# Kernel optimization log

Hardware: AMD Instinct MI355X
Metric: run time of the kernel (lower is better)

Reference implementation:

```python
import jax, jax.numpy as jnp
import numpy as np

B, L, VOCAB = 32768, 512, 50000
CROP_RATIO, MIN_LEN = 0.8, 3
MASK_RATIO, MASK_TOKEN = 0.2, 0
REORDER_RATIO, MIN_W, MAX_W = 0.3, 2, 5


def setup_inputs() -> dict:
    key = jax.random.key(0)
    k1, k2 = jax.random.split(key)
    lens = jax.random.randint(k1, (B,), 1, L + 1)
    items = jax.random.randint(k2, (B, L), 1, VOCAB)
    pos = jnp.arange(L)[None, :]
    item_seq = jnp.where(pos < lens[:, None], items, 0).astype(jnp.int32)
    return {"item_seq": item_seq, "item_seq_len": lens.astype(jnp.int32)}


def _mask_aug(key, seq, lens):
    pos = jnp.arange(seq.shape[1])[None, :]
    valid = (pos < lens[:, None]) & (seq != 0)
    n_valid = valid.sum(axis=1)
    n_mask = jnp.minimum(jnp.maximum(1, (n_valid * MASK_RATIO).astype(jnp.int32)), n_valid)
    scores = jnp.where(valid, jax.random.uniform(key, seq.shape), jnp.inf)
    # rank of each position among valid positions by random score
    rank = jnp.argsort(jnp.argsort(scores, axis=1), axis=1)
    apply_row = (lens > 1) & (n_valid > 0)
    do_mask = valid & (rank < n_mask[:, None]) & apply_row[:, None]
    return jnp.where(do_mask, MASK_TOKEN, seq), lens


def _crop_aug(key, seq, lens):
    Lm = seq.shape[1]
    crop_len = jnp.minimum(jnp.maximum(MIN_LEN, (lens * CROP_RATIO).astype(jnp.int32)), lens)
    max_start = jnp.maximum(lens - crop_len + 1, 1)
    start = (jax.random.uniform(key, (seq.shape[0],)) * max_start).astype(jnp.int32)
    pos = jnp.arange(Lm)[None, :]
    idx = jnp.minimum(start[:, None] + pos, Lm - 1)
    cropped = jnp.where(pos < crop_len[:, None], jnp.take_along_axis(seq, idx, axis=1), 0)
    apply_row = lens > MIN_LEN
    return (jnp.where(apply_row[:, None], cropped, seq),
            jnp.where(apply_row, crop_len, lens))


def _reorder_aug(key, seq, lens):
    Bm, Lm = seq.shape
    k1, k2, k3, k4 = jax.random.split(key, 4)
    pos = jnp.arange(Lm)[None, :]
    valid = (pos < lens[:, None]) & (seq != 0)
    n_valid = valid.sum(axis=1)
    # valid positions first (in order), padding positions after
    valid_idx = jnp.argsort(jnp.where(valid, pos, Lm + pos), axis=1)
    max_w = jnp.minimum(n_valid, MAX_W)
    wsize = MIN_W + (jax.random.uniform(k1, (Bm,)) * jnp.maximum(max_w - MIN_W + 1, 1)).astype(jnp.int32)
    wsize = jnp.clip(wsize, MIN_W, MAX_W)
    max_start = jnp.maximum(n_valid - wsize + 1, 1)
    start = (jax.random.uniform(k2, (Bm,)) * max_start).astype(jnp.int32)
    apply_row = (lens > MIN_W) & (jax.random.uniform(k3, (Bm,)) <= REORDER_RATIO) & (n_valid >= MIN_W)
    k = jnp.arange(MAX_W)[None, :]
    slot_ok = k < wsize[:, None]
    win_cols = jnp.take_along_axis(valid_idx, jnp.minimum(start[:, None] + k, Lm - 1), axis=1)
    win_items = jnp.take_along_axis(seq, win_cols, axis=1)
    # random permutation within the (ragged) window via sorted random keys
    keys = jnp.where(slot_ok, jax.random.uniform(k4, (Bm, MAX_W)), jnp.inf)
    perm = jnp.argsort(keys, axis=1)
    shuffled = jnp.take_along_axis(win_items, perm, axis=1)
    vals = jnp.where(slot_ok & apply_row[:, None], shuffled, win_items)
    rows = jnp.arange(Bm)[:, None]
    return seq.at[rows, win_cols].set(vals), lens


def reference(item_seq, item_seq_len):
    key = jax.random.key(42)
    km, kc, kr = jax.random.split(key, 3)
    mask_seq, mask_len = _mask_aug(km, item_seq, item_seq_len)
    crop_seq, crop_len = _crop_aug(kc, item_seq, item_seq_len)
    reord_seq, reord_len = _reorder_aug(kr, item_seq, item_seq_len)
    return (mask_seq, mask_len, crop_seq, crop_len, reord_seq, reord_len)
```

## Files before the change

### kernel.cpp

```cpp
#include <hip/hip_runtime.h>
#include <stdint.h>


#define NB 32768
#define NL 512
#define NBL (NB * NL)

struct AugKeys {
  uint32_t km0, km1;
  uint32_t kc0, kc1;
  uint32_t r10, r11;
  uint32_t r20, r21;
  uint32_t r30, r31;
  uint32_t r40, r41;
};

__host__ __device__ __forceinline__ uint32_t rotl32(uint32_t x, uint32_t r) {
  return (x << r) | (x >> (32u - r));
}

__host__ __device__ inline void tf2x32(uint32_t k0, uint32_t k1,
                                       uint32_t x0, uint32_t x1,
                                       uint32_t& o0, uint32_t& o1) {
  const uint32_t ks2 = k0 ^ k1 ^ 0x1BD11BDAu;
#define TFR(r) { x0 += x1; x1 = rotl32(x1, r); x1 ^= x0; }
  x0 += k0; x1 += k1;
  TFR(13u) TFR(15u) TFR(26u) TFR(6u)
  x0 += k1; x1 += ks2 + 1u;
  TFR(17u) TFR(29u) TFR(16u) TFR(24u)
  x0 += ks2; x1 += k0 + 2u;
  TFR(13u) TFR(15u) TFR(26u) TFR(6u)
  x0 += k0; x1 += k1 + 3u;
  TFR(17u) TFR(29u) TFR(16u) TFR(24u)
  x0 += k1; x1 += ks2 + 4u;
  TFR(13u) TFR(15u) TFR(26u) TFR(6u)
  x0 += ks2; x1 += k0 + 5u;
#undef TFR
  o0 = x0; o1 = x1;
}

__device__ __forceinline__ float u01f(uint32_t bits) {
  return __uint_as_float((bits >> 9) | 0x3F800000u) - 1.0f;
}

__device__ __forceinline__ uint32_t rbits32(uint32_t k0, uint32_t k1, uint32_t i) {
  uint32_t o0, o1;
  tf2x32(k0, k1, 0u, i, o0, o1);
  return o0 ^ o1;
}

#define SEL8(e, s) \
  (((s) & 4) ? (((s) & 2) ? (((s) & 1) ? e[7] : e[6]) : (((s) & 1) ? e[5] : e[4])) \
             : (((s) & 2) ? (((s) & 1) ? e[3] : e[2]) : (((s) & 1) ? e[1] : e[0])))

__global__ void __launch_bounds__(256)
aug_pipeline(const int* __restrict__ seq, const int* __restrict__ lens,
             int* __restrict__ out, AugKeys K)
{
  __shared__ int s_hist[4][128];
  __shared__ uint32_t s_bin[4][NL];

  const int t = threadIdx.x;
  const int w = t >> 6;
  const int l = t & 63;
  const int b = blockIdx.x * 4 + w;
  const int len = lens[b];
  const int e0 = l * 8;

  const int4 va = reinterpret_cast<const int4*>(seq + (size_t)b * NL)[2 * l];
  const int4 vb = reinterpret_cast<const int4*>(seq + (size_t)b * NL)[2 * l + 1];
  const int elem[8] = {va.x, va.y, va.z, va.w, vb.x, vb.y, vb.z, vb.w};

  uint32_t vmask = 0;
  int nv = 0;
#pragma unroll
  for (int i = 0; i < 8; ++i) {
    const bool vi = (e0 + i < len) && (elem[i] != 0);
    vmask |= (uint32_t)vi << i;
    nv += vi ? 1 : 0;
  }
#pragma unroll
  for (int d = 1; d < 64; d <<= 1) nv += __shfl_xor(nv, d);
  const int n_valid = nv;

  float uval = 0.f;
  if (l < 9) {
    uint32_t kk0, kk1, f;
    if (l == 0)      { kk0 = K.kc0; kk1 = K.kc1; f = (uint32_t)b; }
    else if (l == 1) { kk0 = K.r10; kk1 = K.r11; f = (uint32_t)b; }
    else if (l == 2) { kk0 = K.r20; kk1 = K.r21; f = (uint32_t)b; }
    else if (l == 3) { kk0 = K.r30; kk1 = K.r31; f = (uint32_t)b; }
    else             { kk0 = K.r40; kk1 = K.r41; f = (uint32_t)b * 5u + (uint32_t)(l - 4); }
    uval = u01f(rbits32(kk0, kk1, f));
  }
  const float u_c = __shfl(uval, 0);
  const float u_w = __shfl(uval, 1);
  const float u_s = __shfl(uval, 2);
  const float u_a = __shfl(uval, 3);
  float u4[5];
#pragma unroll
  for (int k = 0; k < 5; ++k) u4[k] = __shfl(uval, 4 + k);

  s_hist[w][2 * l] = 0;
  s_hist[w][2 * l + 1] = 0;
  __builtin_amdgcn_wave_barrier();

  uint32_t key[8];
#pragma unroll
  for (int i = 0; i < 8; ++i) {
    const uint32_t bits = rbits32(K.km0, K.km1, (uint32_t)b * NL + (uint32_t)(e0 + i));
    key[i] = (bits & 0xFFFFFE00u) | (uint32_t)(e0 + i);
    if (vmask & (1u << i)) atomicAdd(&s_hist[w][key[i] >> 25], 1);
  }
  __builtin_amdgcn_wave_barrier();

  const int h0 = s_hist[w][2 * l];
  const int h1 = s_hist[w][2 * l + 1];
  const int pair = h0 + h1;
  int incl = pair;
#pragma unroll
  for (int d = 1; d < 64; d <<= 1) {
    const int o = __shfl_up(incl, d);
    if (l >= d) incl += o;
  }
  const int ex0 = incl - pair;
  const int ex1 = ex0 + h0;
  const int n_mask = min(max(1, (int)((float)n_valid * 0.2f)), n_valid);
  const bool c0 = (h0 > 0) && (ex0 < n_mask) && (n_mask <= ex0 + h0);
  const bool c1 = (h1 > 0) && (ex1 < n_mask) && (n_mask <= ex1 + h1);
  const unsigned long long B0 = __ballot(c0);
  const unsigned long long B1 = __ballot(c1);
  int tbin = -1, below = 0;
  if (B0) {
    const int tl = __ffsll(B0) - 1;
    tbin = 2 * tl; below = __shfl(ex0, tl);
  } else if (B1) {
    const int tl = __ffsll(B1) - 1;
    tbin = 2 * tl + 1; below = __shfl(ex1, tl);
  }
  const int need = n_mask - below;

  int cnt = 0;
  bool inb[8];
#pragma unroll
  for (int i = 0; i < 8; ++i) {
    inb[i] = (vmask & (1u << i)) && ((int)(key[i] >> 25) == tbin);
    cnt += inb[i] ? 1 : 0;
  }
  int cincl = cnt;
#pragma unroll
  for (int d = 1; d < 64; d <<= 1) {
    const int o = __shfl_up(cincl, d);
    if (l >= d) cincl += o;
  }
  const int mtot = __shfl(cincl, 63);
  int off = cincl - cnt;
#pragma unroll
  for (int i = 0; i < 8; ++i) {
    if (inb[i]) s_bin[w][off++] = key[i];
  }
  __builtin_amdgcn_wave_barrier();

  int rk[8] = {0, 0, 0, 0, 0, 0, 0, 0};
  for (int j = 0; j < mtot; ++j) {
    const uint32_t bk = s_bin[w][j];
#pragma unroll
    for (int i = 0; i < 8; ++i) rk[i] += (bk < key[i]) ? 1 : 0;
  }
  const bool apply_m = (len > 1) && (n_valid > 0);
  int o8[8];
#pragma unroll
  for (int i = 0; i < 8; ++i) {
    const int bin = (int)(key[i] >> 25);
    const bool dm = apply_m && (vmask & (1u << i)) && tbin >= 0 &&
                    (bin < tbin || (bin == tbin && rk[i] < need));
    o8[i] = dm ? 0 : elem[i];
  }
  {
    int4* p = reinterpret_cast<int4*>(out + (size_t)b * NL);
    p[2 * l]     = make_int4(o8[0], o8[1], o8[2], o8[3]);
    p[2 * l + 1] = make_int4(o8[4], o8[5], o8[6], o8[7]);
  }

  const int clen = min(max(3, (int)((float)len * 0.8f)), len);
  const int cms = max(len - clen + 1, 1);
  const int cstart = (int)(u_c * (float)cms);
  const bool apply_c = (len > 3);
  int c8[8];
#pragma unroll
  for (int i = 0; i < 8; ++i) {
    const int s = (cstart + i) & 7;
    const int srcl = (cstart + e0 + i) >> 3;
    const int g = __shfl(SEL8(elem, s), srcl);
    c8[i] = apply_c ? ((e0 + i < clen) ? g : 0) : elem[i];
  }
  {
    int4* p = reinterpret_cast<int4*>(out + (size_t)NBL + NB + (size_t)b * NL);
    p[2 * l]     = make_int4(c8[0], c8[1], c8[2], c8[3]);
    p[2 * l + 1] = make_int4(c8[4], c8[5], c8[6], c8[7]);
  }

  const int max_w = min(n_valid, 5);
  int wsize = 2 + (int)(u_w * (float)max(max_w - 1, 1));
  wsize = min(max(wsize, 2), 5);
  const int rms = max(n_valid - wsize + 1, 1);
  const int rstart = (int)(u_s * (float)rms);
  const bool apply_r = (len > 2) && (u_a <= 0.3f) && (n_valid >= 2);

  int cols[5], items[5];
  float fk[5];
#pragma unroll
  for (int k = 0; k < 5; ++k) {
    cols[k] = min(rstart + k, NL - 1);
    const int s = cols[k] & 7;
    items[k] = __shfl(SEL8(elem, s), cols[k] >> 3);
    fk[k] = (k < wsize) ? u4[k] : __int_as_float(0x7F800000);
  }
  int rank5[5];
#pragma unroll
  for (int k = 0; k < 5; ++k) {
    int rr = 0;
#pragma unroll
    for (int j = 0; j < 5; ++j) {
      rr += ((fk[j] < fk[k]) || (fk[j] == fk[k] && j < k)) ? 1 : 0;
    }
    rank5[k] = rr;
  }
  int valk[5];
#pragma unroll
  for (int p = 0; p < 5; ++p) {
    int sh = items[0];
#pragma unroll
    for (int k = 0; k < 5; ++k) if (rank5[k] == p) sh = items[k];
    valk[p] = (apply_r && p < wsize) ? sh : items[p];
  }

  int r8[8] = {elem[0], elem[1], elem[2], elem[3], elem[4], elem[5], elem[6], elem[7]};
#pragma unroll
  for (int k = 0; k < 5; ++k) {
#pragma unroll
    for (int i = 0; i < 8; ++i) if (cols[k] == e0 + i) r8[i] = valk[k];
  }
  {
    int4* p = reinterpret_cast<int4*>(out + 2 * (size_t)NBL + 2 * NB + (size_t)b * NL);
    p[2 * l]     = make_int4(r8[0], r8[1], r8[2], r8[3]);
    p[2 * l + 1] = make_int4(r8[4], r8[5], r8[6], r8[7]);
  }

  if (l == 0) {
    out[(size_t)NBL + b] = len;
    out[2 * (size_t)NBL + NB + b] = apply_c ? clen : len;
    out[3 * (size_t)NBL + 2 * NB + b] = len;
  }
}

extern "C" void kernel_launch(void* const* d_in, const int* in_sizes, int n_in,
                              void* d_out, int out_size, void* d_ws, size_t ws_size,
                              hipStream_t stream) {
  const int* seq  = (const int*)d_in[0];
  const int* lens = (const int*)d_in[1];
  int* out = (int*)d_out;

  AugKeys K;
  uint32_t kr0, kr1;
  tf2x32(0u, 42u, 0u, 0u, K.km0, K.km1);
  tf2x32(0u, 42u, 0u, 1u, K.kc0, K.kc1);
  tf2x32(0u, 42u, 0u, 2u, kr0, kr1);
  tf2x32(kr0, kr1, 0u, 0u, K.r10, K.r11);
  tf2x32(kr0, kr1, 0u, 1u, K.r20, K.r21);
  tf2x32(kr0, kr1, 0u, 2u, K.r30, K.r31);
  tf2x32(kr0, kr1, 0u, 3u, K.r40, K.r41);

  aug_pipeline<<<dim3(NB / 4), dim3(256), 0, stream>>>(seq, lens, out, K);
}
```

Before: 74.32 us.

## Strided threefry key generation to skip RNG work beyond row length

Reassigns mask-key generation so each lane handles positions l, l+64, ... and whole 64-position chunks past the row length are skipped, avoiding threefry evaluations for padding. Valid bits are shared through LDS, the bin scatter uses an LDS atomic counter instead of a prefix scan, and the mask decision is returned to the element-owning lane via ballots stored in shared memory. It also replaces the shuffle reduction for n_valid with ballot popcounts. The trade-off is extra LDS traffic, a per-chunk ballot, and a rank loop that now re-reads the bin list once per chunk rather than once for all keys.

```diff
diff --git a/kernel.cpp b/kernel.cpp
--- a/kernel.cpp
+++ b/kernel.cpp
@@ -59,6 +59,9 @@
 {
   __shared__ int s_hist[4][128];
   __shared__ uint32_t s_bin[4][NL];
+  __shared__ int s_vb[4][64];
+  __shared__ unsigned long long s_D[4][8];
+  __shared__ int s_nbin[4];
 
   const int t = threadIdx.x;
   const int w = t >> 6;
@@ -70,18 +73,6 @@
   const int4 va = reinterpret_cast<const int4*>(seq + (size_t)b * NL)[2 * l];
   const int4 vb = reinterpret_cast<const int4*>(seq + (size_t)b * NL)[2 * l + 1];
   const int elem[8] = {va.x, va.y, va.z, va.w, vb.x, vb.y, vb.z, vb.w};
-
-  uint32_t vmask = 0;
-  int nv = 0;
-#pragma unroll
-  for (int i = 0; i < 8; ++i) {
-    const bool vi = (e0 + i < len) && (elem[i] != 0);
-    vmask |= (uint32_t)vi << i;
-    nv += vi ? 1 : 0;
-  }
-#pragma unroll
-  for (int d = 1; d < 64; d <<= 1) nv += __shfl_xor(nv, d);
-  const int n_valid = nv;
 
   float uval = 0.f;
   if (l < 9) {
@@ -101,16 +92,38 @@
 #pragma unroll
   for (int k = 0; k < 5; ++k) u4[k] = __shfl(uval, 4 + k);
 
+  bool val[8];
+  int vbyte = 0;
+#pragma unroll
+  for (int i = 0; i < 8; ++i) {
+    val[i] = (e0 + i < len) && (elem[i] != 0);
+    vbyte |= (val[i] ? 1 : 0) << i;
+  }
+  int n_valid = 0;
+#pragma unroll
+  for (int i = 0; i < 8; ++i) n_valid += (int)__popcll(__ballot(val[i]));
+
   s_hist[w][2 * l] = 0;
   s_hist[w][2 * l + 1] = 0;
-  __builtin_amdgcn_wave_barrier();
-
-  uint32_t key[8];
-#pragma unroll
-  for (int i = 0; i < 8; ++i) {
-    const uint32_t bits = rbits32(K.km0, K.km1, (uint32_t)b * NL + (uint32_t)(e0 + i));
-    key[i] = (bits & 0xFFFFFE00u) | (uint32_t)(e0 + i);
-    if (vmask & (1u << i)) atomicAdd(&s_hist[w][key[i] >> 25], 1);
+  s_vb[w][l] = vbyte;
+  if (l == 0) s_nbin[w] = 0;
+  __builtin_amdgcn_wave_barrier();
+
+  uint32_t kk[8];
+  uint32_t vsm = 0;
+#pragma unroll
+  for (int it = 0; it < 8; ++it) {
+    if ((it << 6) < len) {
+      const int pos = (it << 6) + l;
+      const uint32_t bits = rbits32(K.km0, K.km1, (uint32_t)b * NL + (uint32_t)pos);
+      kk[it] = (bits & 0xFFFFFE00u) | (uint32_t)pos;
+      const int vb8 = s_vb[w][(it << 3) + (l >> 3)];
+      const bool vs = (vb8 >> (l & 7)) & 1;
+      if (vs) {
+        atomicAdd(&s_hist[w][kk[it] >> 25], 1);
+        vsm |= 1u << it;
+      }
+    }
   }
   __builtin_amdgcn_wave_barrier();
 
@@ -140,41 +153,38 @@
   }
   const int need = n_mask - below;
 
-  int cnt = 0;
-  bool inb[8];
+#pragma unroll
+  for (int it = 0; it < 8; ++it) {
+    if ((it << 6) < len) {
+      if (((vsm >> it) & 1) && (int)(kk[it] >> 25) == tbin) {
+        s_bin[w][atomicAdd(&s_nbin[w], 1)] = kk[it];
+      }
+    }
+  }
+  __builtin_amdgcn_wave_barrier();
+  const int mtot = s_nbin[w];
+  const bool apply_m = (len > 1) && (n_valid > 0);
+
+#pragma unroll
+  for (int it = 0; it < 8; ++it) {
+    if ((it << 6) < len) {
+      int rk = 0;
+      for (int j = 0; j < mtot; ++j) rk += (s_bin[w][j] < kk[it]) ? 1 : 0;
+      const int bin = (int)(kk[it] >> 25);
+      const bool dm = apply_m && ((vsm >> it) & 1) && tbin >= 0 &&
+                      (bin < tbin || (bin == tbin && rk < need));
+      const unsigned long long Dm = __ballot(dm);
+      if (l == 0) s_D[w][it] = Dm;
+    }
+  }
+  __builtin_amdgcn_wave_barrier();
+
+  const unsigned long long Dword = s_D[w][l >> 3];
+  const uint32_t dbyte = (uint32_t)(Dword >> (8 * (l & 7))) & 0xFFu;
+  int o8[8];
 #pragma unroll
   for (int i = 0; i < 8; ++i) {
-    inb[i] = (vmask & (1u << i)) && ((int)(key[i] >> 25) == tbin);
-    cnt += inb[i] ? 1 : 0;
-  }
-  int cincl = cnt;
-#pragma unroll
-  for (int d = 1; d < 64; d <<= 1) {
-    const int o = __shfl_up(cincl, d);
-    if (l >= d) cincl += o;
-  }
-  const int mtot = __shfl(cincl, 63);
-  int off = cincl - cnt;
-#pragma unroll
-  for (int i = 0; i < 8; ++i) {
-    if (inb[i]) s_bin[w][off++] = key[i];
-  }
-  __builtin_amdgcn_wave_barrier();
-
-  int rk[8] = {0, 0, 0, 0, 0, 0, 0, 0};
-  for (int j = 0; j < mtot; ++j) {
-    const uint32_t bk = s_bin[w][j];
-#pragma unroll
-    for (int i = 0; i < 8; ++i) rk[i] += (bk < key[i]) ? 1 : 0;
-  }
-  const bool apply_m = (len > 1) && (n_valid > 0);
-  int o8[8];
-#pragma unroll
-  for (int i = 0; i < 8; ++i) {
-    const int bin = (int)(key[i] >> 25);
-    const bool dm = apply_m && (vmask & (1u << i)) && tbin >= 0 &&
-                    (bin < tbin || (bin == tbin && rk[i] < need));
-    o8[i] = dm ? 0 : elem[i];
+    o8[i] = (val[i] && ((dbyte >> i) & 1)) ? 0 : elem[i];
   }
   {
     int4* p = reinterpret_cast<int4*>(out + (size_t)b * NL);
```

New measurement: 72.48 us. 1.03x faster.
